# Performance work log

Hardware: AMD Instinct MI355X
Metric: run time of the kernel (lower is better)

Reference implementation:

```python
import jax, jax.numpy as jnp
import numpy as np

TN_LAYERS = 2
GCN_LAYERS = 2

def _gru(x, h0, Wih, Whh, bih, bhh):
    # x: (B,T,I), h0: (B,H) -> (B,T,H); torch nn.GRU gate math (r,z,n ordering)
    def step(h, xt):
        gi = xt @ Wih.T + bih
        gh = h @ Whh.T + bhh
        ir, iz, inn = jnp.split(gi, 3, axis=-1)
        hr, hz, hn = jnp.split(gh, 3, axis=-1)
        r = jax.nn.sigmoid(ir + hr)
        z = jax.nn.sigmoid(iz + hz)
        n = jnp.tanh(inn + r * hn)
        h_new = (1.0 - z) * n + z * h
        return h_new, h_new
    _, hs = jax.lax.scan(step, h0, jnp.swapaxes(x, 0, 1))
    return jnp.swapaxes(hs, 0, 1)

def _forward(x, x_mark, sp_emb, sp_W1, sp_b1, sp_W2, sp_b2, t_emb, t_Wih, t_Whh, t_bih, t_bhh,
             gcn_W, gcn_b, fr_W1, fr_b1, fr_W2, fr_b2, tr_Wih, tr_Whh, tr_bih, tr_bhh, out_W, out_b):
    B, T, N = x.shape
    L = sp_b1.shape[0]
    elu = jax.nn.elu
    # --- SpatialEncoder: (B,N,T) ++ static embed -> Linear,ELU,Linear -> (B,N,L)
    xs = jnp.swapaxes(x, 1, 2)
    xs = jnp.concatenate([xs, jnp.broadcast_to(sp_emb, (B,) + sp_emb.shape)], axis=-1)
    Xs = elu(xs @ sp_W1 + sp_b1) @ sp_W2 + sp_b2
    # --- TemporalEncoder: concat(x, x_mark, static time embed) -> GRU -> (B,T,L)
    xt = jnp.concatenate([x, x_mark, jnp.broadcast_to(t_emb, (B,) + t_emb.shape)], axis=-1)
    Xt = _gru(xt, jnp.zeros((B, L), x.dtype), t_Wih, t_Whh, t_bih, t_bhh)
    X = jnp.concatenate([Xs, Xt], axis=1)  # (B, N+T, L)
    # --- TN modules: dynamic adjacency tanh(relu(X X^T)) + weighted message passing.
    # The torch code extracts per-batch sparse edge lists from batch_adj and does
    # gather-weight-scatter over them; zero-weight edges contribute nothing, so this
    # equals dense weighted aggregation A @ X per batch.
    for ti in range(TN_LAYERS):
        A = jnp.tanh(jax.nn.relu(jnp.einsum('bnf,bmf->bnm', X, X)))  # (B,N+T,N+T)
        for li in range(GCN_LAYERS):
            X = elu(jnp.einsum('bnm,bmd->bnd', A, X) @ gcn_W[ti, li] + gcn_b[ti, li])
    # --- Rebuild branches
    Xs2, Xt2 = X[:, :N, :], X[:, N:, :]
    rs = elu(Xs2 @ fr_W1 + fr_b1) @ fr_W2 + fr_b2  # feature_rebuild: (B,N,T)
    rt = _gru(Xt2, jnp.zeros((B, N), x.dtype), tr_Wih, tr_Whh, tr_bih, tr_bhh)  # time_rebuild: (B,T,N)
    combined = rs + jnp.swapaxes(rt, 1, 2)  # (B,N,T)
    return combined @ out_W + out_b  # (B, N, out_seq_len)

def setup_inputs():
    key = jax.random.key(0)
    B, T, N, Dt, L, E = 8, 96, 2000, 4, 32, 32
    ks = iter(jax.random.split(key, 32))
    nrm = lambda shape, s: jax.random.normal(next(ks), shape, jnp.float32) * s
    return {
        'x': nrm((B, T, N), 1.0),
        'x_mark': nrm((B, T, Dt), 1.0),
        'sp_emb': nrm((N, E), 0.1),
        'sp_W1': nrm((T + E, L), (T + E) ** -0.5), 'sp_b1': jnp.zeros((L,), jnp.float32),
        'sp_W2': nrm((L, L), L ** -0.5), 'sp_b2': jnp.zeros((L,), jnp.float32),
        't_emb': nrm((T, E), 0.1),
        't_Wih': nrm((3 * L, N + Dt + E), (N + Dt + E) ** -0.5),
        't_Whh': nrm((3 * L, L), L ** -0.5),
        't_bih': jnp.zeros((3 * L,), jnp.float32), 't_bhh': jnp.zeros((3 * L,), jnp.float32),
        'gcn_W': nrm((TN_LAYERS, GCN_LAYERS, L, L), 3e-3),  # small scale: dense aggregation sums ~N+T terms
        'gcn_b': jnp.zeros((TN_LAYERS, GCN_LAYERS, L), jnp.float32),
        'fr_W1': nrm((L, T), L ** -0.5), 'fr_b1': jnp.zeros((T,), jnp.float32),
        'fr_W2': nrm((T, T), T ** -0.5), 'fr_b2': jnp.zeros((T,), jnp.float32),
        'tr_Wih': nrm((3 * N, L), L ** -0.5), 'tr_Whh': nrm((3 * N, N), N ** -0.5),
        'tr_bih': jnp.zeros((3 * N,), jnp.float32), 'tr_bhh': jnp.zeros((3 * N,), jnp.float32),
        'out_W': nrm((T, 1), T ** -0.5), 'out_b': jnp.zeros((1,), jnp.float32),
    }

def reference(x, x_mark, sp_emb, sp_W1, sp_b1, sp_W2, sp_b2, t_emb, t_Wih, t_Whh, t_bih, t_bhh,
              gcn_W, gcn_b, fr_W1, fr_b1, fr_W2, fr_b2, tr_Wih, tr_Whh, tr_bih, tr_bhh, out_W, out_b):
    return _forward(x, x_mark, sp_emb, sp_W1, sp_b1, sp_W2, sp_b2, t_emb, t_Wih, t_Whh, t_bih, t_bhh,
                    gcn_W, gcn_b, fr_W1, fr_b1, fr_W2, fr_b2, tr_Wih, tr_Whh, tr_bih, tr_bhh, out_W, out_b)
```

## Files before the change

kernel.cpp:

```cpp
#include <hip/hip_runtime.h>

typedef _Float16 half8 __attribute__((ext_vector_type(8)));
typedef float f32x4 __attribute__((ext_vector_type(4)));

#define NBLK 125
#define TOTBLK 250
#define BAR_INTS (TOTBLK * 32)

__global__ __launch_bounds__(256) void k_pre(
    const float* __restrict__ x, const float* __restrict__ x_mark,
    const float* __restrict__ sp_emb,
    const float* __restrict__ spW1, const float* __restrict__ spb1,
    const float* __restrict__ spW2, const float* __restrict__ spb2,
    const float* __restrict__ t_emb, const float* __restrict__ tWih,
    const float* __restrict__ tbih,
    _Float16* __restrict__ X, float* __restrict__ gi,
    int* __restrict__ seq, unsigned char* __restrict__ hA) {
  __shared__ __align__(16) unsigned char PSM[65152];
  int tid = threadIdx.x;
  if (blockIdx.x < 63) {
    float* W1s = (float*)PSM;
    float* W2s = (float*)(PSM + 16384);
    float* b1s = (float*)(PSM + 20480);
    float* b2s = (float*)(PSM + 20608);
    int gidx = blockIdx.x * 256 + tid;
    for (int i = gidx; i < BAR_INTS; i += 63 * 256) seq[i] = 0;
    for (int i = gidx; i < 4000; i += 63 * 256) ((unsigned int*)hA)[i] = 0u;
    for (int i = tid; i < 128 * 32; i += 256) W1s[i] = spW1[i];
    for (int i = tid; i < 32 * 32; i += 256) W2s[i] = spW2[i];
    if (tid < 32) { b1s[tid] = spb1[tid]; b2s[tid] = spb2[tid]; }
    __syncthreads();
    if (gidx >= 8 * 2000) return;
    int b = gidx / 2000, n = gidx % 2000;
    float h1[32];
#pragma unroll
    for (int l = 0; l < 32; l++) h1[l] = b1s[l];
    for (int k = 0; k < 96; k++) {
      float xv = x[((size_t)b * 96 + k) * 2000 + n];
#pragma unroll
      for (int l = 0; l < 32; l++) h1[l] = fmaf(xv, W1s[k * 32 + l], h1[l]);
    }
    for (int e4 = 0; e4 < 8; e4++) {
      float4 ev = *reinterpret_cast<const float4*>(&sp_emb[(size_t)n * 32 + e4 * 4]);
      float evs[4] = {ev.x, ev.y, ev.z, ev.w};
#pragma unroll
      for (int q = 0; q < 4; q++) {
        int e = e4 * 4 + q;
#pragma unroll
        for (int l = 0; l < 32; l++) h1[l] = fmaf(evs[q], W1s[(96 + e) * 32 + l], h1[l]);
      }
    }
    float out[32];
#pragma unroll
    for (int j = 0; j < 32; j++) out[j] = b2s[j];
    for (int l = 0; l < 32; l++) {
      float a = h1[l] > 0.0f ? h1[l] : (__expf(h1[l]) - 1.0f);
#pragma unroll
      for (int j = 0; j < 32; j++) out[j] = fmaf(a, W2s[l * 32 + j], out[j]);
    }
    _Float16* dst = X + ((size_t)b * 2096 + n) * 32;
#pragma unroll
    for (int j8 = 0; j8 < 4; j8++) {
      half8 v;
#pragma unroll
      for (int q = 0; q < 8; q++) v[q] = (_Float16)out[j8 * 8 + q];
      *reinterpret_cast<half8*>(dst + j8 * 8) = v;
    }
  } else {
    float (*xs)[2036] = (float(*)[2036])PSM;
    int row0 = (blockIdx.x - 63) * 8;
    for (int rr = 0; rr < 8; rr++) {
      int row = row0 + rr;
      int b = row / 96, t = row % 96;
      for (int k = tid; k < 2036; k += 256) {
        float v;
        if (k < 2000) v = x[((size_t)b * 96 + t) * 2000 + k];
        else if (k < 2004) v = x_mark[((size_t)b * 96 + t) * 4 + (k - 2000)];
        else v = t_emb[(size_t)t * 32 + (k - 2004)];
        xs[rr][k] = v;
      }
    }
    __syncthreads();
    for (int oi = tid; oi < 8 * 96; oi += 256) {
      int rr = oi & 7, g = oi >> 3;
      const float* w = tWih + (size_t)g * 2036;
      float acc = tbih[g];
      for (int k = 0; k < 2036; k += 4) {
        float4 wv = *reinterpret_cast<const float4*>(w + k);
        acc = fmaf(xs[rr][k + 0], wv.x, acc);
        acc = fmaf(xs[rr][k + 1], wv.y, acc);
        acc = fmaf(xs[rr][k + 2], wv.z, acc);
        acc = fmaf(xs[rr][k + 3], wv.w, acc);
      }
      gi[(size_t)(row0 + rr) * 96 + g] = acc;
    }
  }
}

__global__ __launch_bounds__(768) void k_tgru(
    const float* __restrict__ gi, const float* __restrict__ Whh,
    const float* __restrict__ bhh, _Float16* __restrict__ X) {
  __shared__ float Whs[96][33];
  __shared__ float hs[8][33];
  __shared__ float ga[3][8][33];
  int tid = threadIdx.x;
  for (int i = tid; i < 96 * 32; i += 768) Whs[i >> 5][i & 31] = Whh[i];
  if (tid < 256) hs[tid >> 5][tid & 31] = 0.0f;
  int g = tid >> 8, j = (tid >> 3) & 31, b = tid & 7;
  int row = g * 32 + j;
  float bb0 = 0.f, bb1 = 0.f, bb2 = 0.f;
  if (tid < 256) {
    int jj = tid & 31;
    bb0 = bhh[jj]; bb1 = bhh[32 + jj]; bb2 = bhh[64 + jj];
  }
  __syncthreads();
  for (int t = 0; t < 96; t++) {
    float acc = 0.0f;
#pragma unroll
    for (int k = 0; k < 32; k++) acc = fmaf(hs[b][k], Whs[row][k], acc);
    ga[g][b][j] = acc;
    __syncthreads();
    if (tid < 256) {
      int bb = tid >> 5, jj = tid & 31;
      const float* gp = gi + ((size_t)bb * 96 + t) * 96;
      float gr = ga[0][bb][jj] + bb0;
      float gz = ga[1][bb][jj] + bb1;
      float gn = ga[2][bb][jj] + bb2;
      float r = 1.0f / (1.0f + __expf(-(gp[jj] + gr)));
      float z = 1.0f / (1.0f + __expf(-(gp[32 + jj] + gz)));
      float n = tanhf(gp[64 + jj] + r * gn);
      float hn = (1.0f - z) * n + z * hs[bb][jj];
      hs[bb][jj] = hn;
      X[((size_t)bb * 2096 + 2000 + t) * 32 + jj] = (_Float16)hn;
    }
    __syncthreads();
  }
}

__global__ __launch_bounds__(256) void k_gnn(
    const _Float16* __restrict__ Xa, const _Float16* __restrict__ Xin,
    _Float16* __restrict__ Xout, const float* __restrict__ W,
    const float* __restrict__ bias) {
  __shared__ _Float16 XaR[32][40];
  __shared__ _Float16 Xm[2][64][40];
  __shared__ _Float16 Xq[2][64][42];
  __shared__ _Float16 At[32][72];
  __shared__ float Pm[32][36];
  __shared__ float Ws[32][36];
  __shared__ float bs[32];
  int tid = threadIdx.x;
  int l = tid & 63, w = tid >> 6;
  int b = blockIdx.y;
  int r0 = blockIdx.x * 32;
  const _Float16* Xab = Xa + (size_t)b * 2096 * 32;
  const _Float16* Xib = Xin + (size_t)b * 2096 * 32;
  half8 hz = {(_Float16)0, (_Float16)0, (_Float16)0, (_Float16)0,
              (_Float16)0, (_Float16)0, (_Float16)0, (_Float16)0};

  for (int i = tid; i < 1024; i += 256) Ws[i >> 5][i & 31] = W[i];
  if (tid < 32) bs[tid] = bias[tid];
  if (tid < 128) {
    int r = tid >> 2, k = (tid & 3) * 8;
    half8 v = (r0 + r < 2096)
                  ? *reinterpret_cast<const half8*>(Xab + (size_t)(r0 + r) * 32 + k)
                  : hz;
    *reinterpret_cast<half8*>(&XaR[r][k]) = v;
  }
  int sr = tid >> 2, sk = (tid & 3) * 8;
  {
    *reinterpret_cast<half8*>(&Xm[0][sr][sk]) =
        *reinterpret_cast<const half8*>(Xab + (size_t)sr * 32 + sk);
    half8 vq = *reinterpret_cast<const half8*>(Xib + (size_t)sr * 32 + sk);
    unsigned int u[4];
    __builtin_memcpy(u, &vq, 16);
    unsigned int* qp = (unsigned int*)&Xq[0][sr][sk];
    qp[0] = u[0]; qp[1] = u[1]; qp[2] = u[2]; qp[3] = u[3];
  }
  __syncthreads();

  int lr = l & 15, lk = (l >> 4) * 8, lq = (l >> 4) * 4;
  int smt = w >> 1, snt2 = w & 1;
  int pmt = w >> 1, pnt = w & 1;
  half8 afrag = *reinterpret_cast<const half8*>(&XaR[smt * 16 + lr][lk]);
  f32x4 pacc = {0.f, 0.f, 0.f, 0.f};

  for (int tt = 0; tt < 33; tt++) {
    int cur = tt & 1, nb = cur ^ 1;
    half8 vm = hz, vq = hz;
    bool hv = (tt + 1 < 33);
    if (hv) {
      int gm = (tt + 1) * 64 + sr;
      if (gm < 2096) {
        vm = *reinterpret_cast<const half8*>(Xab + (size_t)gm * 32 + sk);
        vq = *reinterpret_cast<const half8*>(Xib + (size_t)gm * 32 + sk);
      }
    }
#pragma unroll
    for (int n16 = 0; n16 < 2; n16++) {
      int c0 = snt2 * 32 + n16 * 16;
      half8 bfrag = *reinterpret_cast<const half8*>(&Xm[cur][c0 + lr][lk]);
      f32x4 s4 = __builtin_amdgcn_mfma_f32_16x16x32_f16(
          afrag, bfrag, (f32x4){0.f, 0.f, 0.f, 0.f}, 0, 0, 0);
#pragma unroll
      for (int j = 0; j < 4; j++) {
        float e = __expf(-2.0f * fmaxf(s4[j], 0.0f));
        At[smt * 16 + lq + j][c0 + lr] = (_Float16)((1.0f - e) / (1.0f + e));
      }
    }
    __syncthreads();
    {
      int nn = pnt * 16 + lr;
#pragma unroll
      for (int kc = 0; kc < 2; kc++) {
        half8 af = *reinterpret_cast<const half8*>(&At[pmt * 16 + lr][kc * 32 + lk]);
        half8 bf;
        int kb = kc * 32 + lk;
#pragma unroll
        for (int e = 0; e < 8; e++) bf[e] = Xq[cur][kb + e][nn];
        pacc = __builtin_amdgcn_mfma_f32_16x16x32_f16(af, bf, pacc, 0, 0, 0);
      }
    }
    if (hv) {
      *reinterpret_cast<half8*>(&Xm[nb][sr][sk]) = vm;
      unsigned int u[4];
      __builtin_memcpy(u, &vq, 16);
      unsigned int* qp = (unsigned int*)&Xq[nb][sr][sk];
      qp[0] = u[0]; qp[1] = u[1]; qp[2] = u[2]; qp[3] = u[3];
    }
    __syncthreads();
  }

#pragma unroll
  for (int j = 0; j < 4; j++) Pm[pmt * 16 + lq + j][pnt * 16 + lr] = pacc[j];
  __syncthreads();
  int r = tid & 31, fgr = tid >> 5;
  int f0 = fgr * 4;
  float o[4];
#pragma unroll
  for (int j = 0; j < 4; j++) o[j] = bs[f0 + j];
#pragma unroll
  for (int k = 0; k < 32; k++) {
    float mv = Pm[r][k];
    float4 wv = *reinterpret_cast<const float4*>(&Ws[k][f0]);
    o[0] = fmaf(mv, wv.x, o[0]);
    o[1] = fmaf(mv, wv.y, o[1]);
    o[2] = fmaf(mv, wv.z, o[2]);
    o[3] = fmaf(mv, wv.w, o[3]);
  }
  int grr = r0 + r;
  if (grr < 2096) {
    _Float16* dst = Xout + ((size_t)b * 2096 + grr) * 32 + f0;
#pragma unroll
    for (int j = 0; j < 4; j++) {
      float v = o[j];
      dst[j] = (_Float16)(v > 0.0f ? v : (__expf(v) - 1.0f));
    }
  }
}

__global__ __launch_bounds__(1024) void k_trgru(
    const _Float16* __restrict__ X, const float* __restrict__ wih,
    const float* __restrict__ bih, float* __restrict__ gi,
    const float* __restrict__ whh, const float* __restrict__ bhh,
    unsigned char* __restrict__ hA, unsigned char* __restrict__ hB,
    float* __restrict__ rt, int* __restrict__ seq,
    const float* __restrict__ frW1, const float* __restrict__ frb1,
    const float* __restrict__ frW2, const float* __restrict__ frb2,
    float* __restrict__ rs, const float* __restrict__ outW,
    const float* __restrict__ outb, float* __restrict__ out) {
  __shared__ __align__(16) unsigned char SM[122880];
  int tid = threadIdx.x;
  int blk = blockIdx.x;

  if (blk >= NBLK) {
    float* W1s = (float*)(SM);
    float* W2s = (float*)(SM + 12288);
    float* b1s = (float*)(SM + 50688);
    float* b2s = (float*)(SM + 51072);
    float* Xt  = (float*)(SM + 51456);
    float* Hl  = (float*)(SM + 55680);
    for (int i = tid; i < 32 * 96; i += 1024) W1s[i] = frW1[i];
    for (int i = tid; i < 96 * 96; i += 1024) W2s[(i / 96) * 100 + (i % 96)] = frW2[i];
    if (tid < 96) { b1s[tid] = frb1[tid]; b2s[tid] = frb2[tid]; }
    __syncthreads();
    for (int ti = blk - NBLK; ti < 504; ti += NBLK) {
      int b = ti / 63, n0 = (ti % 63) * 32;
      {
        int r = tid >> 5, k = tid & 31;
        Xt[r * 33 + k] =
            (n0 + r < 2000) ? (float)X[((size_t)b * 2096 + n0 + r) * 32 + k] : 0.0f;
      }
      __syncthreads();
#pragma unroll
      for (int q = 0; q < 3; q++) {
        int idx = q * 1024 + tid;
        int r = idx / 96, c = idx % 96;
        float a = b1s[c];
#pragma unroll 8
        for (int k = 0; k < 32; k++) a = fmaf(Xt[r * 33 + k], W1s[k * 96 + c], a);
        Hl[r * 100 + c] = a > 0.0f ? a : (__expf(a) - 1.0f);
      }
      __syncthreads();
#pragma unroll
      for (int q = 0; q < 3; q++) {
        int idx = q * 1024 + tid;
        int r = idx / 96, c = idx % 96;
        float o = b2s[c];
#pragma unroll 8
        for (int k = 0; k < 96; k++) o = fmaf(Hl[r * 100 + k], W2s[k * 100 + c], o);
        if (n0 + r < 2000) {
          __hip_atomic_store(&rs[((size_t)b * 2000 + n0 + r) * 96 + c], o,
                             __ATOMIC_RELAXED, __HIP_MEMORY_SCOPE_AGENT);
        }
      }
      __syncthreads();
    }
    if (tid == 0) {
      __hip_atomic_store(&seq[blk * 32], 96, __ATOMIC_RELAXED,
                         __HIP_MEMORY_SCOPE_AGENT);
    }
  } else {
    unsigned char* wf = SM;
    float* pt = (float*)(SM + 98304);
    int l = tid & 63, w = tid >> 6;

    for (int i = tid; i < 12288; i += 1024) ((unsigned long long*)wf)[i] = 0ull;

    if (tid < 768) {
      int t = tid >> 3, b = tid & 7;
      float xr[32];
      const _Float16* xp = X + ((size_t)b * 2096 + 2000 + t) * 32;
#pragma unroll
      for (int k = 0; k < 32; k++) xr[k] = (float)xp[k];
      float* gp = gi + ((size_t)b * 96 + t) * 6000;
      for (int g = 0; g < 3; g++) {
#pragma unroll
        for (int j = 0; j < 16; j++) {
          int row = g * 2000 + blk * 16 + j;
          const float* wr = wih + (size_t)row * 32;
          float a = bih[row];
#pragma unroll 8
          for (int k = 0; k < 32; k++) a = fmaf(xr[k], wr[k], a);
          gp[row] = a;
        }
      }
    }

    for (int i = tid; i < 3 * 64 * 64; i += 1024) {
      int g = i >> 12;
      int c = (i >> 6) & 63;
      int l2 = i & 63;
      int j = l2 & 15;
      int k0 = c * 32 + ((l2 >> 4) << 3);
      if (k0 <= 1992) {
        const float* src = whh + ((size_t)(g * 2000 + blk * 16 + j)) * 2000 + k0;
        float4 v0 = *reinterpret_cast<const float4*>(src);
        float4 v1 = *reinterpret_cast<const float4*>(src + 4);
        unsigned int lo = __builtin_amdgcn_cvt_pk_fp8_f32(v0.x, v0.y, 0, false);
        lo = __builtin_amdgcn_cvt_pk_fp8_f32(v0.z, v0.w, lo, true);
        unsigned int hi = __builtin_amdgcn_cvt_pk_fp8_f32(v1.x, v1.y, 0, false);
        hi = __builtin_amdgcn_cvt_pk_fp8_f32(v1.z, v1.w, hi, true);
        unsigned long long q = ((unsigned long long)hi << 32) | (unsigned long long)lo;
        *reinterpret_cast<unsigned long long*>(wf + (size_t)g * 32768 + c * 512 + l2 * 8) = q;
      }
    }

    int cj = tid >> 3, cb = tid & 7;
    int jg = blk * 16 + cj;
    float hold = 0.0f, bR = 0.f, bZ = 0.f, bN = 0.f;
    if (tid < 128) {
      bR = bhh[jg]; bZ = bhh[2000 + jg]; bN = bhh[4000 + jg];
    }
    int bb = l & 7, kblk = (l >> 4) * 8;
    __syncthreads();

    float gir = 0.f, giz = 0.f, gin = 0.f;
    if (tid < 128) {
      const float* gp = gi + ((size_t)cb * 96 + 0) * 6000;
      gir = gp[jg]; giz = gp[2000 + jg]; gin = gp[4000 + jg];
    }

    for (int t = 0; t < 96; t++) {
      const unsigned char* hc = (t & 1) ? hB : hA;
      unsigned char* hn = (t & 1) ? hA : hB;
      f32x4 a0 = {0.f, 0.f, 0.f, 0.f}, a1 = {0.f, 0.f, 0.f, 0.f}, a2 = {0.f, 0.f, 0.f, 0.f};
#pragma unroll
      for (int i = 0; i < 4; i++) {
        int c = w * 4 + i;
        int k0 = c * 32 + kblk;
        long long bv = 0;
        if (k0 <= 1992)
          bv = *reinterpret_cast<const long long*>(hc + bb * 2000 + k0);
        long long w0 = *reinterpret_cast<const long long*>(wf + 0 * 32768 + c * 512 + l * 8);
        long long w1 = *reinterpret_cast<const long long*>(wf + 1 * 32768 + c * 512 + l * 8);
        long long w2 = *reinterpret_cast<const long long*>(wf + 2 * 32768 + c * 512 + l * 8);
        a0 = __builtin_amdgcn_mfma_f32_16x16x32_fp8_fp8(w0, bv, a0, 0, 0, 0);
        a1 = __builtin_amdgcn_mfma_f32_16x16x32_fp8_fp8(w1, bv, a1, 0, 0, 0);
        a2 = __builtin_amdgcn_mfma_f32_16x16x32_fp8_fp8(w2, bv, a2, 0, 0, 0);
      }
      {
        int bcol = l & 15;
        if (bcol < 8) {
          int lb = l >> 4;
          *reinterpret_cast<f32x4*>(pt + w * 384 + 0 * 128 + lb * 32 + bcol * 4) = a0;
          *reinterpret_cast<f32x4*>(pt + w * 384 + 1 * 128 + lb * 32 + bcol * 4) = a1;
          *reinterpret_cast<f32x4*>(pt + w * 384 + 2 * 128 + lb * 32 + bcol * 4) = a2;
        }
      }
      __syncthreads();
      if (tid < 128) {
        float s[3];
#pragma unroll
        for (int g = 0; g < 3; g++) {
          int base = g * 128 + (cj >> 2) * 32 + cb * 4 + (cj & 3);
          float acc = 0.f;
#pragma unroll
          for (int w2 = 0; w2 < 16; w2++) acc += pt[w2 * 384 + base];
          s[g] = acc;
        }
        float r_ = 1.0f / (1.0f + __expf(-(gir + s[0] + bR)));
        float z_ = 1.0f / (1.0f + __expf(-(giz + s[1] + bZ)));
        float n_ = tanhf(gin + r_ * (s[2] + bN));
        hold = (1.0f - z_) * n_ + z_ * hold;
        {
          unsigned int p = __builtin_amdgcn_cvt_pk_fp8_f32(hold, 0.0f, 0, false);
          __hip_atomic_store(hn + cb * 2000 + jg, (unsigned char)(p & 0xFF),
                             __ATOMIC_RELAXED, __HIP_MEMORY_SCOPE_AGENT);
        }
        __hip_atomic_store(&rt[((size_t)cb * 96 + t) * 2000 + jg], hold,
                           __ATOMIC_RELAXED, __HIP_MEMORY_SCOPE_AGENT);
      }
      __syncthreads();
      if (tid == 0) {
        __hip_atomic_store(&seq[blk * 32], t + 1, __ATOMIC_RELAXED,
                           __HIP_MEMORY_SCOPE_AGENT);
      }
      if (tid < 128 && t + 1 < 96) {
        const float* gp = gi + ((size_t)cb * 96 + (t + 1)) * 6000;
        gir = gp[jg]; giz = gp[2000 + jg]; gin = gp[4000 + jg];
      }
      if ((tid >> 6) == 2) {
        int lane = tid & 63;
        const int* s1 = &seq[lane * 32];
        const int* s2 = &seq[((lane + 64) < NBLK ? (lane + 64) : lane) * 32];
        while (true) {
          int v1 = __hip_atomic_load(s1, __ATOMIC_RELAXED, __HIP_MEMORY_SCOPE_AGENT);
          int v2 = __hip_atomic_load(s2, __ATOMIC_RELAXED, __HIP_MEMORY_SCOPE_AGENT);
          if (__all(v1 > t && v2 > t)) break;
          __builtin_amdgcn_s_sleep(1);
        }
        if (lane == 0) {
          (void)__hip_atomic_load(s1, __ATOMIC_ACQUIRE, __HIP_MEMORY_SCOPE_AGENT);
        }
      }
      __syncthreads();
    }
  }

  {
    float* wsm = (float*)SM;
    __syncthreads();
    if (tid >= 128 && tid < 224) wsm[tid - 128] = outW[tid - 128];
    if (tid == 224) wsm[96] = outb[0];
    if (tid < 64) {
      const int* p0 = &seq[tid * 32];
      const int* p1 = &seq[(tid + 64) * 32];
      const int* p2 = &seq[(tid + 128) * 32];
      int i3 = tid + 192; if (i3 >= TOTBLK) i3 = tid;
      const int* p3 = &seq[i3 * 32];
      while (true) {
        int v0 = __hip_atomic_load(p0, __ATOMIC_RELAXED, __HIP_MEMORY_SCOPE_AGENT);
        int v1 = __hip_atomic_load(p1, __ATOMIC_RELAXED, __HIP_MEMORY_SCOPE_AGENT);
        int v2 = __hip_atomic_load(p2, __ATOMIC_RELAXED, __HIP_MEMORY_SCOPE_AGENT);
        int v3 = __hip_atomic_load(p3, __ATOMIC_RELAXED, __HIP_MEMORY_SCOPE_AGENT);
        if (__all(v0 >= 96 && v1 >= 96 && v2 >= 96 && v3 >= 96)) break;
        __builtin_amdgcn_s_sleep(2);
      }
      if (tid == 0) {
        (void)__hip_atomic_load(p0, __ATOMIC_ACQUIRE, __HIP_MEMORY_SCOPE_AGENT);
      }
    }
    __syncthreads();
    if (tid < 64) {
      int idx = blk * 64 + tid;
      int b = idx / 2000, n = idx % 2000;
      const float* rsp = rs + (size_t)idx * 96;
      float acc = wsm[96];
      for (int t4 = 0; t4 < 24; t4++) {
        float4 rv = *reinterpret_cast<const float4*>(rsp + t4 * 4);
        int t = t4 * 4;
        acc = fmaf(rv.x + rt[((size_t)b * 96 + t + 0) * 2000 + n], wsm[t + 0], acc);
        acc = fmaf(rv.y + rt[((size_t)b * 96 + t + 1) * 2000 + n], wsm[t + 1], acc);
        acc = fmaf(rv.z + rt[((size_t)b * 96 + t + 2) * 2000 + n], wsm[t + 2], acc);
        acc = fmaf(rv.w + rt[((size_t)b * 96 + t + 3) * 2000 + n], wsm[t + 3], acc);
      }
      out[idx] = acc;
    }
  }
}

extern "C" void kernel_launch(void* const* d_in, const int* in_sizes, int n_in,
                              void* d_out, int out_size, void* d_ws, size_t ws_size,
                              hipStream_t stream) {
  const float* x      = (const float*)d_in[0];
  const float* x_mark = (const float*)d_in[1];
  const float* sp_emb = (const float*)d_in[2];
  const float* sp_W1  = (const float*)d_in[3];
  const float* sp_b1  = (const float*)d_in[4];
  const float* sp_W2  = (const float*)d_in[5];
  const float* sp_b2  = (const float*)d_in[6];
  const float* t_emb  = (const float*)d_in[7];
  const float* t_Wih  = (const float*)d_in[8];
  const float* t_Whh  = (const float*)d_in[9];
  const float* t_bih  = (const float*)d_in[10];
  const float* t_bhh  = (const float*)d_in[11];
  const float* gcn_W  = (const float*)d_in[12];
  const float* gcn_b  = (const float*)d_in[13];
  const float* fr_W1  = (const float*)d_in[14];
  const float* fr_b1  = (const float*)d_in[15];
  const float* fr_W2  = (const float*)d_in[16];
  const float* fr_b2  = (const float*)d_in[17];
  const float* tr_Wih = (const float*)d_in[18];
  const float* tr_Whh = (const float*)d_in[19];
  const float* tr_bih = (const float*)d_in[20];
  const float* tr_bhh = (const float*)d_in[21];
  const float* out_W  = (const float*)d_in[22];
  const float* out_b  = (const float*)d_in[23];
  (void)in_sizes; (void)n_in; (void)out_size; (void)ws_size;

  float* ws = (float*)d_ws;
  float* X0   = ws;
  float* X1   = X0 + 536576;
  float* X2   = X1 + 536576;
  float* tgi  = X2 + 536576;
  float* trgi = tgi + 73728;
  float* hsl  = trgi + 4608000;
  float* rt   = hsl + 16000;
  float* rs   = rt + 1536000;
  float* barf = rs + 1536000;

  _Float16* X0h = (_Float16*)X0;
  _Float16* X1h = (_Float16*)X1;
  _Float16* X2h = (_Float16*)X2;
  unsigned char* hA = (unsigned char*)hsl;
  unsigned char* hB = hA + 16000;
  int* seq = (int*)barf;

  k_pre<<<159, 256, 0, stream>>>(x, x_mark, sp_emb, sp_W1, sp_b1, sp_W2, sp_b2,
                                 t_emb, t_Wih, t_bih, X0h, tgi, seq, hA);
  k_tgru<<<1, 768, 0, stream>>>(tgi, t_Whh, t_bhh, X0h);

  dim3 gg(66, 8);
  k_gnn<<<gg, 256, 0, stream>>>(X0h, X0h, X1h, gcn_W + 0 * 1024, gcn_b + 0 * 32);
  k_gnn<<<gg, 256, 0, stream>>>(X0h, X1h, X2h, gcn_W + 1 * 1024, gcn_b + 1 * 32);
  k_gnn<<<gg, 256, 0, stream>>>(X2h, X2h, X0h, gcn_W + 2 * 1024, gcn_b + 2 * 32);
  k_gnn<<<gg, 256, 0, stream>>>(X2h, X0h, X1h, gcn_W + 3 * 1024, gcn_b + 3 * 32);

  {
    const _Float16* a0 = X1h;
    const float* a1 = tr_Wih;
    const float* a2 = tr_bih;
    float* a3 = trgi;
    const float* a4 = tr_Whh;
    const float* a5 = tr_bhh;
    unsigned char* a6 = hA;
    unsigned char* a7 = hB;
    float* a8 = rt;
    int* a9 = seq;
    const float* a10 = fr_W1;
    const float* a11 = fr_b1;
    const float* a12 = fr_W2;
    const float* a13 = fr_b2;
    float* a14 = rs;
    const float* a15 = out_W;
    const float* a16 = out_b;
    float* a17 = (float*)d_out;
    void* cargs[] = {&a0, &a1, &a2, &a3, &a4, &a5, &a6, &a7, &a8, &a9,
                     &a10, &a11, &a12, &a13, &a14, &a15, &a16, &a17};
    hipLaunchCooperativeKernel((const void*)k_trgru, dim3(TOTBLK), dim3(1024), cargs, 0, stream);
  }
}
```

Measured before the change: 908.2 us.

## Fuse four GNN layer launches into one cooperative kernel with grid flag barriers

Replaces the four separate k_gnn launches with a single cooperative persistent kernel (528 blocks) that runs all four message-passing layers. Between layers, each block publishes a per-block flag and spins until all blocks reach the phase, which acts as a software grid barrier. The aim is to remove kernel launch gaps and tail effects between layers. The cost is spin-wait overhead, extra flag memory, and a requirement that all 528 blocks be co-resident; if the cooperative launch fails, it falls back to the old launches.

```diff
diff --git a/kernel.cpp b/kernel.cpp
--- a/kernel.cpp
+++ b/kernel.cpp
@@ -5,7 +5,8 @@
 
 #define NBLK 125
 #define TOTBLK 250
-#define BAR_INTS (TOTBLK * 32)
+#define GNNUNITS 528
+#define BAR_INTS (8192 + GNNUNITS * 32)
 
 __global__ __launch_bounds__(256) void k_pre(
     const float* __restrict__ x, const float* __restrict__ x_mark,
@@ -254,6 +255,177 @@
     for (int j = 0; j < 4; j++) {
       float v = o[j];
       dst[j] = (_Float16)(v > 0.0f ? v : (__expf(v) - 1.0f));
+    }
+  }
+}
+
+__global__ __launch_bounds__(256, 4) void k_gnnmega(
+    _Float16* __restrict__ X0, _Float16* __restrict__ X1, _Float16* __restrict__ X2,
+    const float* __restrict__ gcnW, const float* __restrict__ gcnb,
+    int* __restrict__ seqbase) {
+  __shared__ _Float16 XaR[32][40];
+  __shared__ _Float16 Xm[2][64][40];
+  __shared__ _Float16 Xq[2][64][42];
+  __shared__ _Float16 At[32][72];
+  __shared__ float Pm[32][36];
+  __shared__ float Ws[32][36];
+  __shared__ float bs[32];
+  int tid = threadIdx.x;
+  int blk = blockIdx.x;
+  int* gflags = seqbase + 8192;
+
+  const _Float16* gXa[4] = {X0, X0, X2, X2};
+  const _Float16* gXi[4] = {X0, X1, X2, X0};
+  _Float16* gXo[4] = {X1, X2, X0, X1};
+  half8 hz = {(_Float16)0, (_Float16)0, (_Float16)0, (_Float16)0,
+              (_Float16)0, (_Float16)0, (_Float16)0, (_Float16)0};
+
+  int ub = blk / 66, ux = blk % 66;
+  int r0 = ux * 32;
+  int l = tid & 63, w = tid >> 6;
+  int lr = l & 15, lk = (l >> 4) * 8, lq = (l >> 4) * 4;
+  int smt = w >> 1, snt2 = w & 1;
+  int pmt = w >> 1, pnt = w & 1;
+  int sr = tid >> 2, sk = (tid & 3) * 8;
+
+  for (int p = 0; p < 4; p++) {
+    const _Float16* Xab = gXa[p] + (size_t)ub * 2096 * 32;
+    const _Float16* Xib = gXi[p] + (size_t)ub * 2096 * 32;
+    _Float16* Xob = gXo[p] + (size_t)ub * 2096 * 32;
+    const float* W = gcnW + p * 1024;
+    const float* bias = gcnb + p * 32;
+
+    for (int i = tid; i < 1024; i += 256) Ws[i >> 5][i & 31] = W[i];
+    if (tid < 32) bs[tid] = bias[tid];
+    if (tid < 128) {
+      int r = tid >> 2, k = (tid & 3) * 8;
+      half8 v = (r0 + r < 2096)
+                    ? *reinterpret_cast<const half8*>(Xab + (size_t)(r0 + r) * 32 + k)
+                    : hz;
+      *reinterpret_cast<half8*>(&XaR[r][k]) = v;
+    }
+    {
+      *reinterpret_cast<half8*>(&Xm[0][sr][sk]) =
+          *reinterpret_cast<const half8*>(Xab + (size_t)sr * 32 + sk);
+      half8 vq = *reinterpret_cast<const half8*>(Xib + (size_t)sr * 32 + sk);
+      unsigned int u[4];
+      __builtin_memcpy(u, &vq, 16);
+      unsigned int* qp = (unsigned int*)&Xq[0][sr][sk];
+      qp[0] = u[0]; qp[1] = u[1]; qp[2] = u[2]; qp[3] = u[3];
+    }
+    __syncthreads();
+
+    half8 afrag = *reinterpret_cast<const half8*>(&XaR[smt * 16 + lr][lk]);
+    f32x4 pacc = {0.f, 0.f, 0.f, 0.f};
+
+    for (int tt = 0; tt < 33; tt++) {
+      int cur = tt & 1, nb = cur ^ 1;
+      half8 vm = hz, vq = hz;
+      bool hv = (tt + 1 < 33);
+      if (hv) {
+        int gm = (tt + 1) * 64 + sr;
+        if (gm < 2096) {
+          vm = *reinterpret_cast<const half8*>(Xab + (size_t)gm * 32 + sk);
+          vq = *reinterpret_cast<const half8*>(Xib + (size_t)gm * 32 + sk);
+        }
+      }
+#pragma unroll
+      for (int n16 = 0; n16 < 2; n16++) {
+        int c0 = snt2 * 32 + n16 * 16;
+        half8 bfrag = *reinterpret_cast<const half8*>(&Xm[cur][c0 + lr][lk]);
+        f32x4 s4 = __builtin_amdgcn_mfma_f32_16x16x32_f16(
+            afrag, bfrag, (f32x4){0.f, 0.f, 0.f, 0.f}, 0, 0, 0);
+#pragma unroll
+        for (int j = 0; j < 4; j++) {
+          float e = __expf(-2.0f * fmaxf(s4[j], 0.0f));
+          At[smt * 16 + lq + j][c0 + lr] = (_Float16)((1.0f - e) / (1.0f + e));
+        }
+      }
+      __syncthreads();
+      {
+        int nn = pnt * 16 + lr;
+#pragma unroll
+        for (int kc = 0; kc < 2; kc++) {
+          half8 af = *reinterpret_cast<const half8*>(&At[pmt * 16 + lr][kc * 32 + lk]);
+          half8 bf;
+          int kb = kc * 32 + lk;
+#pragma unroll
+          for (int e = 0; e < 8; e++) bf[e] = Xq[cur][kb + e][nn];
+          pacc = __builtin_amdgcn_mfma_f32_16x16x32_f16(af, bf, pacc, 0, 0, 0);
+        }
+      }
+      if (hv) {
+        *reinterpret_cast<half8*>(&Xm[nb][sr][sk]) = vm;
+        unsigned int u[4];
+        __builtin_memcpy(u, &vq, 16);
+        unsigned int* qp = (unsigned int*)&Xq[nb][sr][sk];
+        qp[0] = u[0]; qp[1] = u[1]; qp[2] = u[2]; qp[3] = u[3];
+      }
+      __syncthreads();
+    }
+
+#pragma unroll
+    for (int j = 0; j < 4; j++) Pm[pmt * 16 + lq + j][pnt * 16 + lr] = pacc[j];
+    __syncthreads();
+    {
+      int r = tid & 31, fgr = tid >> 5;
+      int f0 = fgr * 4;
+      float o[4];
+#pragma unroll
+      for (int j = 0; j < 4; j++) o[j] = bs[f0 + j];
+#pragma unroll
+      for (int k = 0; k < 32; k++) {
+        float mv = Pm[r][k];
+        float4 wv = *reinterpret_cast<const float4*>(&Ws[k][f0]);
+        o[0] = fmaf(mv, wv.x, o[0]);
+        o[1] = fmaf(mv, wv.y, o[1]);
+        o[2] = fmaf(mv, wv.z, o[2]);
+        o[3] = fmaf(mv, wv.w, o[3]);
+      }
+      int grr = r0 + r;
+      if (grr < 2096) {
+#pragma unroll
+        for (int j = 0; j < 4; j++) {
+          float v = o[j];
+          o[j] = v > 0.0f ? v : (__expf(v) - 1.0f);
+        }
+        _Float16 h0 = (_Float16)o[0], h1v = (_Float16)o[1];
+        _Float16 h2 = (_Float16)o[2], h3 = (_Float16)o[3];
+        unsigned short u0, u1, u2, u3;
+        __builtin_memcpy(&u0, &h0, 2); __builtin_memcpy(&u1, &h1v, 2);
+        __builtin_memcpy(&u2, &h2, 2); __builtin_memcpy(&u3, &h3, 2);
+        unsigned int* dst = (unsigned int*)(Xob + (size_t)grr * 32 + f0);
+        __hip_atomic_store(dst, ((unsigned int)u1 << 16) | u0, __ATOMIC_RELAXED,
+                           __HIP_MEMORY_SCOPE_AGENT);
+        __hip_atomic_store(dst + 1, ((unsigned int)u3 << 16) | u2, __ATOMIC_RELAXED,
+                           __HIP_MEMORY_SCOPE_AGENT);
+      }
+    }
+    __syncthreads();
+    if (p < 3) {
+      if (tid == 0)
+        __hip_atomic_store(&gflags[blk * 32], p + 1, __ATOMIC_RELAXED,
+                           __HIP_MEMORY_SCOPE_AGENT);
+      if (tid < 64) {
+        while (true) {
+          bool ok = true;
+#pragma unroll
+          for (int q = 0; q < 9; q++) {
+            int idx = tid + 64 * q;
+            if (idx < GNNUNITS) {
+              int v = __hip_atomic_load(&gflags[idx * 32], __ATOMIC_RELAXED,
+                                        __HIP_MEMORY_SCOPE_AGENT);
+              if (v < p + 1) ok = false;
+            }
+          }
+          if (__all(ok)) break;
+          __builtin_amdgcn_s_sleep(2);
+        }
+        if (tid == 0)
+          (void)__hip_atomic_load(&gflags[0], __ATOMIC_ACQUIRE,
+                                  __HIP_MEMORY_SCOPE_AGENT);
+      }
+      __syncthreads();
     }
   }
 }
@@ -550,11 +722,23 @@
                                  t_emb, t_Wih, t_bih, X0h, tgi, seq, hA);
   k_tgru<<<1, 768, 0, stream>>>(tgi, t_Whh, t_bhh, X0h);
 
-  dim3 gg(66, 8);
-  k_gnn<<<gg, 256, 0, stream>>>(X0h, X0h, X1h, gcn_W + 0 * 1024, gcn_b + 0 * 32);
-  k_gnn<<<gg, 256, 0, stream>>>(X0h, X1h, X2h, gcn_W + 1 * 1024, gcn_b + 1 * 32);
-  k_gnn<<<gg, 256, 0, stream>>>(X2h, X2h, X0h, gcn_W + 2 * 1024, gcn_b + 2 * 32);
-  k_gnn<<<gg, 256, 0, stream>>>(X2h, X0h, X1h, gcn_W + 3 * 1024, gcn_b + 3 * 32);
+  {
+    _Float16* a0 = X0h; _Float16* a1 = X1h; _Float16* a2 = X2h;
+    const float* a3 = gcn_W;
+    const float* a4 = gcn_b;
+    int* a5 = seq;
+    void* cargs[] = {&a0, &a1, &a2, &a3, &a4, &a5};
+    hipError_t e = hipLaunchCooperativeKernel((const void*)k_gnnmega, dim3(GNNUNITS),
+                                              dim3(256), cargs, 0, stream);
+    if (e != hipSuccess) {
+      (void)hipGetLastError();
+      dim3 gg(66, 8);
+      k_gnn<<<gg, 256, 0, stream>>>(X0h, X0h, X1h, gcn_W + 0 * 1024, gcn_b + 0 * 32);
+      k_gnn<<<gg, 256, 0, stream>>>(X0h, X1h, X2h, gcn_W + 1 * 1024, gcn_b + 1 * 32);
+      k_gnn<<<gg, 256, 0, stream>>>(X2h, X2h, X0h, gcn_W + 2 * 1024, gcn_b + 2 * 32);
+      k_gnn<<<gg, 256, 0, stream>>>(X2h, X0h, X1h, gcn_W + 3 * 1024, gcn_b + 3 * 32);
+    }
+  }
 
   {
     const _Float16* a0 = X1h;
```

After: 948.4 us. +4.4%, slower.
